# Performance work log

Hardware: AMD Instinct MI355X
Metric: run time of the kernel (lower is better)

## Reference

```python
import jax, jax.numpy as jnp
import numpy as np

B = 131072  # batch of chess positions


def _window_idx():
    # For window i: x=i//6, y=i%6; gather 3x3 squares, 6 features each -> 54 cols
    idx = np.zeros((36, 54), dtype=np.int32)
    for i in range(36):
        x, y = i // 6, i % 6
        cols = []
        for ox in range(3):
            for oy in range(3):
                base = (x + ox) * 8 * 6 + (y + oy) * 6
                cols.extend(range(base, base + 6))
        idx[i] = cols
    return jnp.asarray(idx)

_IDX = _window_idx()  # [36, 54]


def crelu(x):
    return jnp.clip(x, -1.0, 1.0)


def setup_inputs() -> dict:
    key = jax.random.key(0)
    ks = jax.random.split(key, 13)
    s = 0.3  # weight scale
    return {
        "inp": jax.random.normal(ks[0], (B, 385), dtype=jnp.float32),
        "W1": jax.random.normal(ks[1], (54, 12), dtype=jnp.float32) * s,
        "b1": jax.random.normal(ks[2], (12,), dtype=jnp.float32) * s,
        "W2": jax.random.normal(ks[3], (12, 12), dtype=jnp.float32) * s,
        "b2": jax.random.normal(ks[4], (12,), dtype=jnp.float32) * s,
        "W3": jax.random.normal(ks[5], (12, 4), dtype=jnp.float32) * s,
        "b3": jax.random.normal(ks[6], (4,), dtype=jnp.float32) * s,
        "V1": jax.random.normal(ks[7], (145, 32), dtype=jnp.float32) * s,
        "c1": jax.random.normal(ks[8], (32,), dtype=jnp.float32) * s,
        "V2": jax.random.normal(ks[9], (32, 32), dtype=jnp.float32) * s,
        "c2": jax.random.normal(ks[10], (32,), dtype=jnp.float32) * s,
        "V3": jax.random.normal(ks[11], (32, 1), dtype=jnp.float32) * s,
        "c3": jax.random.normal(ks[12], (1,), dtype=jnp.float32) * s,
    }


def reference(inp, W1, b1, W2, b2, W3, b3, V1, c1, V2, c2, V3, c3):
    b = inp.shape[0]
    win = inp[:, _IDX]                               # [B, 36, 54] im2col gather
    h = crelu(jnp.einsum("bwk,kn->bwn", win, W1) + b1)   # [B, 36, 12]
    h = crelu(h @ W2 + b2)                           # [B, 36, 12]
    sight = crelu(h @ W3 + b3)                       # [B, 36, 4]
    vision = jnp.concatenate([sight.reshape(b, 144), inp[:, 384:385]], axis=1)  # [B,145]
    e = crelu(vision @ V1 + c1)                      # [B, 32]
    e = crelu(e @ V2 + c2)                           # [B, 32]
    return crelu(e @ V3 + c3)                        # [B, 1]
```

## Files before the change

kernel.cpp:

```cpp
#include <hip/hip_runtime.h>

#define NT   384
#define SPB  32
#define LSTR 386
#define LPAD 64

#define WS_V2_OFF 2560
#define WS_SLOTS  3072
#define WS_LC_GROUPS 11

typedef __attribute__((ext_vector_type(4))) float     f32x4;
typedef __attribute__((ext_vector_type(8))) _Float16  f16x8;
typedef __attribute__((ext_vector_type(4))) _Float16  f16x4;

union U8 { f16x8 v; unsigned u[4]; uint4 q; };
union U4 { f16x4 v; unsigned u[2]; };

static __device__ inline unsigned pack_f16(float a, float b) {
    union { _Float16 h[2]; unsigned u; } c;
    c.h[0] = (_Float16)a; c.h[1] = (_Float16)b;
    return c.u;
}
static __device__ inline void split_pack(float a, float b, unsigned& hi, unsigned& lo) {
    const _Float16 ah = (_Float16)a, bh = (_Float16)b;
    hi = pack_f16((float)ah, (float)bh);
    lo = pack_f16(a - (float)ah, b - (float)bh);
}
static __device__ inline unsigned short to_f16u(float a) {
    union { _Float16 h; unsigned short u; } c;
    c.h = (_Float16)a;
    return c.u;
}
static __device__ inline float clamp1(float v) { return fminf(fmaxf(v, -1.f), 1.f); }

static __device__ inline f32x4 mfma32(f16x8 a, f16x8 b, f32x4 c) {
    return __builtin_amdgcn_mfma_f32_16x16x32_f16(a, b, c, 0, 0, 0);
}
static __device__ inline f32x4 mfma16(f16x4 a, f16x4 b, f32x4 c) {
#if __has_builtin(__builtin_amdgcn_mfma_f32_16x16x16f16)
    return __builtin_amdgcn_mfma_f32_16x16x16f16(a, b, c, 0, 0, 0);
#else
    f32x4 d;
    asm volatile("v_mfma_f32_16x16x16_f16 %0, %1, %2, %3\n\ts_nop 7\n\ts_nop 1"
                 : "=v"(d) : "v"(a), "v"(b), "v"(c));
    return d;
#endif
}

__global__ void lila_pack(const float* __restrict__ W1, const float* __restrict__ b1,
                          const float* __restrict__ W2, const float* __restrict__ b2,
                          const float* __restrict__ W3, const float* __restrict__ b3,
                          const float* __restrict__ V1, const float* __restrict__ V2,
                          uint2* __restrict__ ws)
{
    const int i = blockIdx.x * 256 + threadIdx.x;
    if (i < WS_SLOTS) {
        float a, b;
        if (i < WS_V2_OFF) {
            const int p = i >> 5, n = i & 31;
            a = (2 * p     < 145) ? V1[(2 * p)     * 32 + n] : 0.f;
            b = (2 * p + 1 < 145) ? V1[(2 * p + 1) * 32 + n] : 0.f;
        } else {
            const int j = i - WS_V2_OFF, p = j >> 5, n = j & 31;
            a = V2[(2 * p)     * 32 + n];
            b = V2[(2 * p + 1) * 32 + n];
        }
        uint2 t;
        split_pack(a, b, t.x, t.y);
        ws[i] = t;
    } else if (i < WS_SLOTS + 64) {
        const int lid  = i - WS_SLOTS;
        const int quad = lid >> 4, c16 = lid & 15;
        uint4* lc = (uint4*)(ws + WS_SLOTS);
        for (int f = 0; f < 2; ++f) {
            unsigned hu[4], lu[4];
            for (int j2 = 0; j2 < 4; ++j2) {
                const int k0 = f * 32 + quad * 8 + 2 * j2;
                const float v0 = (k0     < 54 && c16 < 12) ? W1[k0 * 12 + c16]       : 0.f;
                const float v1 = (k0 + 1 < 54 && c16 < 12) ? W1[(k0 + 1) * 12 + c16] : 0.f;
                split_pack(v0, v1, hu[j2], lu[j2]);
            }
            lc[(0 + f) * 64 + lid] = make_uint4(hu[0], hu[1], hu[2], hu[3]);
            lc[(2 + f) * 64 + lid] = make_uint4(lu[0], lu[1], lu[2], lu[3]);
        }
        {
            unsigned h2[2], l2[2], h3[2], l3[2];
            for (int j2 = 0; j2 < 2; ++j2) {
                const int k0 = quad * 4 + 2 * j2;
                const float a0 = (k0     < 12 && c16 < 12) ? W2[k0 * 12 + c16]       : 0.f;
                const float a1 = (k0 + 1 < 12 && c16 < 12) ? W2[(k0 + 1) * 12 + c16] : 0.f;
                split_pack(a0, a1, h2[j2], l2[j2]);
                const float g0 = (k0     < 12 && c16 < 4) ? W3[k0 * 4 + c16]       : 0.f;
                const float g1 = (k0 + 1 < 12 && c16 < 4) ? W3[(k0 + 1) * 4 + c16] : 0.f;
                split_pack(g0, g1, h3[j2], l3[j2]);
            }
            lc[4 * 64 + lid] = make_uint4(h2[0], h2[1], l2[0], l2[1]);
            lc[5 * 64 + lid] = make_uint4(h3[0], h3[1], l3[0], l3[1]);
        }
        {
            unsigned q1[4], q2[4], q3[4];
            for (int r = 0; r < 4; ++r) {
                const int c = quad * 4 + r;
                q1[r] = __float_as_uint((c < 12) ? b1[c] : 0.f);
                q2[r] = __float_as_uint((c < 12) ? b2[c] : 0.f);
                q3[r] = __float_as_uint((c < 4)  ? b3[c] : 0.f);
            }
            lc[6 * 64 + lid] = make_uint4(q1[0], q1[1], q1[2], q1[3]);
            lc[7 * 64 + lid] = make_uint4(q2[0], q2[1], q2[2], q2[3]);
            lc[8 * 64 + lid] = make_uint4(q3[0], q3[1], q3[2], q3[3]);
        }
        {
            unsigned d[8];
            for (int p = 0; p < 8; ++p) {
                const int k = (p >> 2) * 32 + quad * 8 + 2 * (p & 3);
                d[p] = (unsigned)((k / 18) * 48 + (k % 18));
            }
            lc[9  * 64 + lid] = make_uint4(d[0], d[1], d[2], d[3]);
            lc[10 * 64 + lid] = make_uint4(d[4], d[5], d[6], d[7]);
        }
    }
}

__global__ __launch_bounds__(NT, 4)
void lila_fused(const float* __restrict__ inp,
                const float* __restrict__ c1, const float* __restrict__ c2,
                const float* __restrict__ V3, const float* __restrict__ c3,
                const uint2* __restrict__ wpk,
                float* __restrict__ out)
{
    __shared__ __align__(16) unsigned short lbuf16[SPB * LSTR + LPAD];
    __shared__ __align__(16) uint2 vis[80 * 32];

    uint2* le1u = (uint2*)lbuf16;

    const int tid  = threadIdx.x;
    const int lid  = tid & 63;
    const int wv   = tid >> 6;
    const int quad = lid >> 4;
    const int c16  = lid & 15;
    const int s0   = blockIdx.x * SPB;

    const uint4* lc = (const uint4*)(wpk + WS_SLOTS);
    U8 wa1h[2], wa1l[2];
    wa1h[0].q = lc[0 * 64 + lid];
    wa1h[1].q = lc[1 * 64 + lid];
    wa1l[0].q = lc[2 * 64 + lid];
    wa1l[1].q = lc[3 * 64 + lid];
    const uint4 t4 = lc[4 * 64 + lid], t5 = lc[5 * 64 + lid];
    U4 wa2h, wa2l, wa3h, wa3l;
    wa2h.u[0] = t4.x; wa2h.u[1] = t4.y; wa2l.u[0] = t4.z; wa2l.u[1] = t4.w;
    wa3h.u[0] = t5.x; wa3h.u[1] = t5.y; wa3l.u[0] = t5.z; wa3l.u[1] = t5.w;
    const uint4 t6 = lc[6 * 64 + lid], t7 = lc[7 * 64 + lid], t8 = lc[8 * 64 + lid];
    const float b1v[4] = {__uint_as_float(t6.x), __uint_as_float(t6.y),
                          __uint_as_float(t6.z), __uint_as_float(t6.w)};
    const float b2v[4] = {__uint_as_float(t7.x), __uint_as_float(t7.y),
                          __uint_as_float(t7.z), __uint_as_float(t7.w)};
    const float b3v[4] = {__uint_as_float(t8.x), __uint_as_float(t8.y),
                          __uint_as_float(t8.z), __uint_as_float(t8.w)};
    const uint4 t9 = lc[9 * 64 + lid], tA = lc[10 * 64 + lid];
    const int dofs[8] = {(int)t9.x, (int)t9.y, (int)t9.z, (int)t9.w,
                         (int)tA.x, (int)tA.y, (int)tA.z, (int)tA.w};

    {
        const float* g = inp + (size_t)s0 * 385;
        #pragma unroll 4
        for (int r = 0; r < SPB; ++r)
            lbuf16[r * LSTR + tid] = to_f16u(g[r * 385 + tid]);
        if (tid < 64)        lbuf16[(tid >> 1) * LSTR + 384 + (tid & 1)] = 0;
        else if (tid < 128)  lbuf16[SPB * LSTR + (tid - 64)] = 0;
        if (tid < 256) {
            const int p = 72 + (tid >> 5);
            const int s = tid & 31;
            uint2 t; t.x = 0u; t.y = 0u;
            if (p == 72) {
                const float lv = g[s * 385 + 384];
                split_pack(lv, 0.f, t.x, t.y);
            }
            vis[p * 32 + (s & 16) + (((s & 15) + p) & 15)] = t;
        }
    }
    __syncthreads();

    const f32x4 z = {0.f, 0.f, 0.f, 0.f};
    for (int t = wv; t < (SPB * 36) / 16; t += NT / 64) {
        const int r = t * 16 + c16;
        const int s = r / 36;
        const int w = r - s * 36;
        const int x = w / 6;
        const int y = w - x * 6;
        const int base = s * LSTR + x * 48 + y * 6;

        U8 bw[2];
        #pragma unroll
        for (int p = 0; p < 8; ++p)
            bw[p >> 2].u[p & 3] = *(const unsigned*)(&lbuf16[base + dofs[p]]);

        f32x4 acc = z;
        acc = mfma32(wa1h[0].v, bw[0].v, acc);
        acc = mfma32(wa1h[1].v, bw[1].v, acc);
        acc = mfma32(wa1l[0].v, bw[0].v, acc);
        acc = mfma32(wa1l[1].v, bw[1].v, acc);

        U4 bb2;
        bb2.u[0] = pack_f16(clamp1(acc[0] + b1v[0]), clamp1(acc[1] + b1v[1]));
        bb2.u[1] = pack_f16(clamp1(acc[2] + b1v[2]), clamp1(acc[3] + b1v[3]));
        f32x4 d2 = mfma16(wa2h.v, bb2.v, z);
        d2 = mfma16(wa2l.v, bb2.v, d2);

        U4 bb3;
        bb3.u[0] = pack_f16(clamp1(d2[0] + b2v[0]), clamp1(d2[1] + b2v[1]));
        bb3.u[1] = pack_f16(clamp1(d2[2] + b2v[2]), clamp1(d2[3] + b2v[3]));
        f32x4 d3 = mfma16(wa3h.v, bb3.v, z);
        d3 = mfma16(wa3l.v, bb3.v, d3);

        if (lid < 16) {
            const float v0 = clamp1(d3[0] + b3v[0]);
            const float v1 = clamp1(d3[1] + b3v[1]);
            const float v2 = clamp1(d3[2] + b3v[2]);
            const float v3 = clamp1(d3[3] + b3v[3]);
            unsigned h01, l01, h23, l23;
            split_pack(v0, v1, h01, l01);
            split_pack(v2, v3, h23, l23);
            const int p0 = 2 * w;
            uint2 t0; t0.x = h01; t0.y = l01;
            uint2 t1; t1.x = h23; t1.y = l23;
            vis[p0       * 32 + (s & 16) + (((s & 15) + p0    ) & 15)] = t0;
            vis[(p0 + 1) * 32 + (s & 16) + (((s & 15) + p0 + 1) & 15)] = t1;
        }
    }
    __syncthreads();

    if (wv < 4) {
        const int sh = wv >> 1, nt = wv & 1;
        f32x4 acc = z;
        #pragma unroll
        for (int kk = 0; kk < 5; ++kk) {
            U8 ah, al, bh, bl;
            #pragma unroll
            for (int j2 = 0; j2 < 4; ++j2) {
                const int p = kk * 16 + quad * 4 + j2;
                const uint2 a = wpk[p * 32 + nt * 16 + c16];
                ah.u[j2] = a.x; al.u[j2] = a.y;
                const uint2 b = vis[p * 32 + sh * 16 + ((c16 + p) & 15)];
                bh.u[j2] = b.x; bl.u[j2] = b.y;
            }
            acc = mfma32(al.v, bl.v, acc);
            acc = mfma32(al.v, bh.v, acc);
            acc = mfma32(ah.v, bl.v, acc);
            acc = mfma32(ah.v, bh.v, acc);
        }
        const float4 c1v = *(const float4*)(c1 + nt * 16 + quad * 4);
        const float e0 = clamp1(acc[0] + c1v.x);
        const float e1 = clamp1(acc[1] + c1v.y);
        const float e2 = clamp1(acc[2] + c1v.z);
        const float e3 = clamp1(acc[3] + c1v.w);
        unsigned h01, l01, h23, l23;
        split_pack(e0, e1, h01, l01);
        split_pack(e2, e3, h23, l23);
        const int p0 = nt * 8 + quad * 2;
        uint2 t0; t0.x = h01; t0.y = l01;
        uint2 t1; t1.x = h23; t1.y = l23;
        le1u[p0       * 32 + sh * 16 + ((c16 + p0    ) & 15)] = t0;
        le1u[(p0 + 1) * 32 + sh * 16 + ((c16 + p0 + 1) & 15)] = t1;
    }
    __syncthreads();

    if (wv < 2) {
        const int sh = wv;
        float part = 0.f;
        #pragma unroll
        for (int nt2 = 0; nt2 < 2; ++nt2) {
            U8 ah, al, bh, bl;
            #pragma unroll
            for (int j2 = 0; j2 < 4; ++j2) {
                const int p = quad * 4 + j2;
                const uint2 a = wpk[WS_V2_OFF + p * 32 + nt2 * 16 + c16];
                ah.u[j2] = a.x; al.u[j2] = a.y;
                const uint2 b = le1u[p * 32 + sh * 16 + ((c16 + p) & 15)];
                bh.u[j2] = b.x; bl.u[j2] = b.y;
            }
            f32x4 d = z;
            d = mfma32(al.v, bl.v, d);
            d = mfma32(al.v, bh.v, d);
            d = mfma32(ah.v, bl.v, d);
            d = mfma32(ah.v, bh.v, d);
            const float4 c2v = *(const float4*)(c2 + nt2 * 16 + quad * 4);
            const float4 v3v = *(const float4*)(V3 + nt2 * 16 + quad * 4);
            part += clamp1(d[0] + c2v.x) * v3v.x + clamp1(d[1] + c2v.y) * v3v.y
                  + clamp1(d[2] + c2v.z) * v3v.z + clamp1(d[3] + c2v.w) * v3v.w;
        }
        part += __shfl_xor(part, 16);
        part += __shfl_xor(part, 32);
        if (lid < 16)
            out[s0 + sh * 16 + c16] = clamp1(part + c3[0]);
    }
}

extern "C" void kernel_launch(void* const* d_in, const int* in_sizes, int n_in,
                              void* d_out, int out_size, void* d_ws, size_t ws_size,
                              hipStream_t stream) {
    const float* inp = (const float*)d_in[0];
    const float* W1  = (const float*)d_in[1];
    const float* b1  = (const float*)d_in[2];
    const float* W2  = (const float*)d_in[3];
    const float* b2  = (const float*)d_in[4];
    const float* W3  = (const float*)d_in[5];
    const float* b3  = (const float*)d_in[6];
    const float* V1  = (const float*)d_in[7];
    const float* c1  = (const float*)d_in[8];
    const float* V2  = (const float*)d_in[9];
    const float* c2  = (const float*)d_in[10];
    const float* V3  = (const float*)d_in[11];
    const float* c3  = (const float*)d_in[12];
    float* out = (float*)d_out;

    uint2* wpk = (uint2*)d_ws;
    lila_pack<<<dim3((WS_SLOTS + 64 + 255) / 256), dim3(256), 0, stream>>>(
        W1, b1, W2, b2, W3, b3, V1, V2, wpk);

    const int Btot   = in_sizes[0] / 385;
    const int blocks = Btot / SPB;

    lila_fused<<<dim3(blocks), dim3(NT), 0, stream>>>(
        inp, c1, c2, V3, c3, wpk, out);
}
```

Measured before the change: 337.2 us.

## Drop low-half activation splits, fold biases into MFMA accumulators, raise occupancy

Intermediate activations (sight, e1) are now stored only as single fp16 values rather than hi/lo pairs. This halves the shared-memory footprint for vis/le1 and removes half of the V1/V2 MFMAs; the lone residual feature is handled through an extra packed V1 row. Biases now seed the MFMA accumulators instead of being added afterwards, clamp uses fmed3, and launch bounds go from 4 to 6 waves per SIMD. The cost is lower precision on the activations, and the tighter launch bounds could cause register spills.

```diff
diff --git a/kernel.cpp b/kernel.cpp
--- a/kernel.cpp
+++ b/kernel.cpp
@@ -4,10 +4,10 @@
 #define SPB  32
 #define LSTR 386
 #define LPAD 64
+#define VSTR 34
 
 #define WS_V2_OFF 2560
 #define WS_SLOTS  3072
-#define WS_LC_GROUPS 11
 
 typedef __attribute__((ext_vector_type(4))) float     f32x4;
 typedef __attribute__((ext_vector_type(8))) _Float16  f16x8;
@@ -31,7 +31,7 @@
     c.h = (_Float16)a;
     return c.u;
 }
-static __device__ inline float clamp1(float v) { return fminf(fmaxf(v, -1.f), 1.f); }
+static __device__ inline float clamp1(float v) { return __builtin_amdgcn_fmed3f(v, -1.f, 1.f); }
 
 static __device__ inline f32x4 mfma32(f16x8 a, f16x8 b, f32x4 c) {
     return __builtin_amdgcn_mfma_f32_16x16x32_f16(a, b, c, 0, 0, 0);
@@ -58,7 +58,8 @@
         float a, b;
         if (i < WS_V2_OFF) {
             const int p = i >> 5, n = i & 31;
-            a = (2 * p     < 145) ? V1[(2 * p)     * 32 + n] : 0.f;
+            a = (2 * p < 145) ? V1[(2 * p) * 32 + n]
+                              : ((p == 73) ? V1[144 * 32 + n] : 0.f);
             b = (2 * p + 1 < 145) ? V1[(2 * p + 1) * 32 + n] : 0.f;
         } else {
             const int j = i - WS_V2_OFF, p = j >> 5, n = j & 31;
@@ -121,7 +122,7 @@
     }
 }
 
-__global__ __launch_bounds__(NT, 4)
+__global__ __launch_bounds__(NT, 6)
 void lila_fused(const float* __restrict__ inp,
                 const float* __restrict__ c1, const float* __restrict__ c2,
                 const float* __restrict__ V3, const float* __restrict__ c3,
@@ -129,9 +130,9 @@
                 float* __restrict__ out)
 {
     __shared__ __align__(16) unsigned short lbuf16[SPB * LSTR + LPAD];
-    __shared__ __align__(16) uint2 vis[80 * 32];
-
-    uint2* le1u = (uint2*)lbuf16;
+    __shared__ __align__(16) unsigned vis[80 * VSTR];
+
+    unsigned* le1u = (unsigned*)lbuf16;
 
     const int tid  = threadIdx.x;
     const int lid  = tid & 63;
@@ -151,12 +152,12 @@
     wa2h.u[0] = t4.x; wa2h.u[1] = t4.y; wa2l.u[0] = t4.z; wa2l.u[1] = t4.w;
     wa3h.u[0] = t5.x; wa3h.u[1] = t5.y; wa3l.u[0] = t5.z; wa3l.u[1] = t5.w;
     const uint4 t6 = lc[6 * 64 + lid], t7 = lc[7 * 64 + lid], t8 = lc[8 * 64 + lid];
-    const float b1v[4] = {__uint_as_float(t6.x), __uint_as_float(t6.y),
-                          __uint_as_float(t6.z), __uint_as_float(t6.w)};
-    const float b2v[4] = {__uint_as_float(t7.x), __uint_as_float(t7.y),
-                          __uint_as_float(t7.z), __uint_as_float(t7.w)};
-    const float b3v[4] = {__uint_as_float(t8.x), __uint_as_float(t8.y),
-                          __uint_as_float(t8.z), __uint_as_float(t8.w)};
+    const f32x4 accb1 = {__uint_as_float(t6.x), __uint_as_float(t6.y),
+                         __uint_as_float(t6.z), __uint_as_float(t6.w)};
+    const f32x4 accb2 = {__uint_as_float(t7.x), __uint_as_float(t7.y),
+                         __uint_as_float(t7.z), __uint_as_float(t7.w)};
+    const f32x4 accb3 = {__uint_as_float(t8.x), __uint_as_float(t8.y),
+                         __uint_as_float(t8.z), __uint_as_float(t8.w)};
     const uint4 t9 = lc[9 * 64 + lid], tA = lc[10 * 64 + lid];
     const int dofs[8] = {(int)t9.x, (int)t9.y, (int)t9.z, (int)t9.w,
                          (int)tA.x, (int)tA.y, (int)tA.z, (int)tA.w};
@@ -171,17 +172,17 @@
         if (tid < 256) {
             const int p = 72 + (tid >> 5);
             const int s = tid & 31;
-            uint2 t; t.x = 0u; t.y = 0u;
-            if (p == 72) {
+            unsigned t = 0u;
+            if (p < 74) {
                 const float lv = g[s * 385 + 384];
-                split_pack(lv, 0.f, t.x, t.y);
-            }
-            vis[p * 32 + (s & 16) + (((s & 15) + p) & 15)] = t;
+                if (p == 72) t = pack_f16(lv, 0.f);
+                else         t = pack_f16(lv - (float)(_Float16)lv, 0.f);
+            }
+            vis[p * VSTR + (s & 16) + (((s & 15) + p) & 15)] = t;
         }
     }
     __syncthreads();
 
-    const f32x4 z = {0.f, 0.f, 0.f, 0.f};
     for (int t = wv; t < (SPB * 36) / 16; t += NT / 64) {
         const int r = t * 16 + c16;
         const int s = r / 36;
@@ -195,73 +196,58 @@
         for (int p = 0; p < 8; ++p)
             bw[p >> 2].u[p & 3] = *(const unsigned*)(&lbuf16[base + dofs[p]]);
 
-        f32x4 acc = z;
+        f32x4 acc = accb1;
         acc = mfma32(wa1h[0].v, bw[0].v, acc);
         acc = mfma32(wa1h[1].v, bw[1].v, acc);
         acc = mfma32(wa1l[0].v, bw[0].v, acc);
         acc = mfma32(wa1l[1].v, bw[1].v, acc);
 
         U4 bb2;
-        bb2.u[0] = pack_f16(clamp1(acc[0] + b1v[0]), clamp1(acc[1] + b1v[1]));
-        bb2.u[1] = pack_f16(clamp1(acc[2] + b1v[2]), clamp1(acc[3] + b1v[3]));
-        f32x4 d2 = mfma16(wa2h.v, bb2.v, z);
+        bb2.u[0] = pack_f16(clamp1(acc[0]), clamp1(acc[1]));
+        bb2.u[1] = pack_f16(clamp1(acc[2]), clamp1(acc[3]));
+        f32x4 d2 = accb2;
+        d2 = mfma16(wa2h.v, bb2.v, d2);
         d2 = mfma16(wa2l.v, bb2.v, d2);
 
         U4 bb3;
-        bb3.u[0] = pack_f16(clamp1(d2[0] + b2v[0]), clamp1(d2[1] + b2v[1]));
-        bb3.u[1] = pack_f16(clamp1(d2[2] + b2v[2]), clamp1(d2[3] + b2v[3]));
-        f32x4 d3 = mfma16(wa3h.v, bb3.v, z);
+        bb3.u[0] = pack_f16(clamp1(d2[0]), clamp1(d2[1]));
+        bb3.u[1] = pack_f16(clamp1(d2[2]), clamp1(d2[3]));
+        f32x4 d3 = accb3;
+        d3 = mfma16(wa3h.v, bb3.v, d3);
         d3 = mfma16(wa3l.v, bb3.v, d3);
 
         if (lid < 16) {
-            const float v0 = clamp1(d3[0] + b3v[0]);
-            const float v1 = clamp1(d3[1] + b3v[1]);
-            const float v2 = clamp1(d3[2] + b3v[2]);
-            const float v3 = clamp1(d3[3] + b3v[3]);
-            unsigned h01, l01, h23, l23;
-            split_pack(v0, v1, h01, l01);
-            split_pack(v2, v3, h23, l23);
+            const unsigned h01 = pack_f16(clamp1(d3[0]), clamp1(d3[1]));
+            const unsigned h23 = pack_f16(clamp1(d3[2]), clamp1(d3[3]));
             const int p0 = 2 * w;
-            uint2 t0; t0.x = h01; t0.y = l01;
-            uint2 t1; t1.x = h23; t1.y = l23;
-            vis[p0       * 32 + (s & 16) + (((s & 15) + p0    ) & 15)] = t0;
-            vis[(p0 + 1) * 32 + (s & 16) + (((s & 15) + p0 + 1) & 15)] = t1;
+            vis[p0       * VSTR + (s & 16) + (((s & 15) + p0    ) & 15)] = h01;
+            vis[(p0 + 1) * VSTR + (s & 16) + (((s & 15) + p0 + 1) & 15)] = h23;
         }
     }
     __syncthreads();
 
     if (wv < 4) {
         const int sh = wv >> 1, nt = wv & 1;
-        f32x4 acc = z;
+        const float4 c1v = *(const float4*)(c1 + nt * 16 + quad * 4);
+        f32x4 acc = {c1v.x, c1v.y, c1v.z, c1v.w};
         #pragma unroll
         for (int kk = 0; kk < 5; ++kk) {
-            U8 ah, al, bh, bl;
+            U8 ah, al, bh;
             #pragma unroll
             for (int j2 = 0; j2 < 4; ++j2) {
                 const int p = kk * 16 + quad * 4 + j2;
                 const uint2 a = wpk[p * 32 + nt * 16 + c16];
                 ah.u[j2] = a.x; al.u[j2] = a.y;
-                const uint2 b = vis[p * 32 + sh * 16 + ((c16 + p) & 15)];
-                bh.u[j2] = b.x; bl.u[j2] = b.y;
-            }
-            acc = mfma32(al.v, bl.v, acc);
+                bh.u[j2] = vis[p * VSTR + sh * 16 + ((c16 + p) & 15)];
+            }
             acc = mfma32(al.v, bh.v, acc);
-            acc = mfma32(ah.v, bl.v, acc);
             acc = mfma32(ah.v, bh.v, acc);
         }
-        const float4 c1v = *(const float4*)(c1 + nt * 16 + quad * 4);
-        const float e0 = clamp1(acc[0] + c1v.x);
-        const float e1 = clamp1(acc[1] + c1v.y);
-        const float e2 = clamp1(acc[2] + c1v.z);
-        const float e3 = clamp1(acc[3] + c1v.w);
-        unsigned h01, l01, h23, l23;
-        split_pack(e0, e1, h01, l01);
-        split_pack(e2, e3, h23, l23);
+        const unsigned h01 = pack_f16(clamp1(acc[0]), clamp1(acc[1]));
+        const unsigned h23 = pack_f16(clamp1(acc[2]), clamp1(acc[3]));
         const int p0 = nt * 8 + quad * 2;
-        uint2 t0; t0.x = h01; t0.y = l01;
-        uint2 t1; t1.x = h23; t1.y = l23;
-        le1u[p0       * 32 + sh * 16 + ((c16 + p0    ) & 15)] = t0;
-        le1u[(p0 + 1) * 32 + sh * 16 + ((c16 + p0 + 1) & 15)] = t1;
+        le1u[p0       * VSTR + sh * 16 + ((c16 + p0    ) & 15)] = h01;
+        le1u[(p0 + 1) * VSTR + sh * 16 + ((c16 + p0 + 1) & 15)] = h23;
     }
     __syncthreads();
 
@@ -270,24 +256,21 @@
         float part = 0.f;
         #pragma unroll
         for (int nt2 = 0; nt2 < 2; ++nt2) {
-            U8 ah, al, bh, bl;
+            U8 ah, al, bh;
             #pragma unroll
             for (int j2 = 0; j2 < 4; ++j2) {
                 const int p = quad * 4 + j2;
                 const uint2 a = wpk[WS_V2_OFF + p * 32 + nt2 * 16 + c16];
                 ah.u[j2] = a.x; al.u[j2] = a.y;
-                const uint2 b = le1u[p * 32 + sh * 16 + ((c16 + p) & 15)];
-                bh.u[j2] = b.x; bl.u[j2] = b.y;
-            }
-            f32x4 d = z;
-            d = mfma32(al.v, bl.v, d);
+                bh.u[j2] = le1u[p * VSTR + sh * 16 + ((c16 + p) & 15)];
+            }
+            const float4 c2v = *(const float4*)(c2 + nt2 * 16 + quad * 4);
+            f32x4 d = {c2v.x, c2v.y, c2v.z, c2v.w};
             d = mfma32(al.v, bh.v, d);
-            d = mfma32(ah.v, bl.v, d);
             d = mfma32(ah.v, bh.v, d);
-            const float4 c2v = *(const float4*)(c2 + nt2 * 16 + quad * 4);
             const float4 v3v = *(const float4*)(V3 + nt2 * 16 + quad * 4);
-            part += clamp1(d[0] + c2v.x) * v3v.x + clamp1(d[1] + c2v.y) * v3v.y
-                  + clamp1(d[2] + c2v.z) * v3v.z + clamp1(d[3] + c2v.w) * v3v.w;
+            part += clamp1(d[0]) * v3v.x + clamp1(d[1]) * v3v.y
+                  + clamp1(d[2]) * v3v.z + clamp1(d[3]) * v3v.w;
         }
         part += __shfl_xor(part, 16);
         part += __shfl_xor(part, 32);
```

Result: faster. 325.2 us (-3.5%).
